# Kernel optimization log

Measured on AMD Instinct MI355X. Metric: run time of the kernel, lower is better.

Reference implementation:

```python
import jax, jax.numpy as jnp
import numpy as np

THRESH = 0.5      # jaccard_thresh
NEGPOS = 3        # neg:pos ratio for hard negative mining
VAR0, VAR1 = 0.1, 0.2  # SSD encoding variances


def point_form(boxes):
    # center-size [P,4] -> (xmin,ymin,xmax,ymax)
    return jnp.concatenate([boxes[:, :2] - boxes[:, 2:] / 2,
                            boxes[:, :2] + boxes[:, 2:] / 2], axis=1)


def jaccard(box_a, box_b):
    # box_a [O,4], box_b [P,4] point-form -> IoU [O,P]
    lt = jnp.maximum(box_a[:, None, :2], box_b[None, :, :2])
    rb = jnp.minimum(box_a[:, None, 2:], box_b[None, :, 2:])
    wh = jnp.clip(rb - lt, 0.0)
    inter = wh[..., 0] * wh[..., 1]
    area_a = ((box_a[:, 2] - box_a[:, 0]) * (box_a[:, 3] - box_a[:, 1]))[:, None]
    area_b = ((box_b[:, 2] - box_b[:, 0]) * (box_b[:, 3] - box_b[:, 1]))[None, :]
    return inter / (area_a + area_b - inter)


def encode(matched, priors):
    # matched point-form [P,4], priors center-size [P,4]
    g_cxcy = ((matched[:, :2] + matched[:, 2:]) / 2 - priors[:, :2]) / (VAR0 * priors[:, 2:])
    g_wh = jnp.log((matched[:, 2:] - matched[:, :2]) / priors[:, 2:]) / VAR1
    return jnp.concatenate([g_cxcy, g_wh], axis=1)


def match_one(truths, labels, priors):
    # truths [O,4] point-form, labels [O] int, priors [P,4] center-size
    O = truths.shape[0]
    ov = jaccard(truths, point_form(priors))          # [O,P]
    best_prior_idx = jnp.argmax(ov, axis=1)           # [O]
    best_truth_ov = jnp.max(ov, axis=0)               # [P]
    best_truth_idx = jnp.argmax(ov, axis=0)           # [P]
    # ensure each gt matches its best prior
    best_truth_ov = best_truth_ov.at[best_prior_idx].set(2.0)
    best_truth_idx = best_truth_idx.at[best_prior_idx].set(jnp.arange(O))
    matches = truths[best_truth_idx]                  # [P,4]
    conf = jnp.where(best_truth_ov < THRESH, 0, labels[best_truth_idx] + 1)
    return encode(matches, priors), conf


def setup_inputs() -> dict:
    key = jax.random.key(0)
    ks = jax.random.split(key, 6)
    B, P, C, O = 32, 24656, 81, 16
    predictions = jax.random.normal(ks[0], (B, P, 4 + C), dtype=jnp.float32)
    # priors: center-size, valid w/h
    pc = jax.random.uniform(ks[1], (P, 2), minval=0.05, maxval=0.95)
    pwh = jax.random.uniform(ks[2], (P, 2), minval=0.02, maxval=0.3)
    priors = jnp.concatenate([pc, pwh], axis=1).astype(jnp.float32)
    # ground-truth boxes in point form, guaranteed positive extent
    tc = jax.random.uniform(ks[3], (B, O, 2), minval=0.2, maxval=0.8)
    twh = jax.random.uniform(ks[4], (B, O, 2), minval=0.05, maxval=0.3)
    targets_boxes = jnp.concatenate([tc - twh / 2, tc + twh / 2], axis=-1).astype(jnp.float32)
    targets_labels = jax.random.randint(ks[5], (B, O), 0, C - 1, dtype=jnp.int32)
    return {"predictions": predictions, "targets_boxes": targets_boxes,
            "targets_labels": targets_labels, "priors": priors}


def reference(predictions, targets_boxes, targets_labels, priors):
    loc_data = predictions[..., :4]        # [B,P,4]
    conf_data = predictions[..., 4:]       # [B,P,C]
    B, P = loc_data.shape[:2]
    C = conf_data.shape[2]

    loc_t, conf_t = jax.vmap(match_one, in_axes=(0, 0, None))(
        targets_boxes, targets_labels, priors)   # [B,P,4], [B,P]

    pos = conf_t > 0                                   # [B,P]
    # smooth L1 on positives, sum reduction
    d = loc_data - loc_t
    ad = jnp.abs(d)
    sl1 = jnp.where(ad < 1.0, 0.5 * d * d, ad - 0.5)
    loss_l = jnp.sum(sl1 * pos[..., None].astype(sl1.dtype))

    # per-anchor cross entropy
    logp = jax.nn.log_softmax(conf_data, axis=-1)
    lbl = jnp.clip(conf_t, 0, C - 1)
    ce = -jnp.take_along_axis(logp, lbl[..., None], axis=-1)[..., 0]  # [B,P]

    # hard negative mining: rank negatives by loss (positives zeroed)
    loss_rank = jnp.where(pos, 0.0, ce)
    loss_idx = jnp.argsort(-loss_rank, axis=1)
    idx_rank = jnp.argsort(loss_idx, axis=1)
    num_pos = jnp.sum(pos, axis=1, keepdims=True)          # [B,1]
    num_neg = jnp.minimum(num_pos * NEGPOS, P)
    neg = idx_rank < num_neg

    sel = (pos | neg).astype(ce.dtype)
    loss_c = jnp.sum(ce * sel)

    N = jnp.sum(num_pos).astype(loss_l.dtype)
    return loss_l / N, loss_c / N
```

## Files before the change

kernel.cpp:

```cpp
#include <hip/hip_runtime.h>
#include <math.h>

#define NB 32
#define NP 24656
#define NO 16
#define NC 81
#define ND 85
#define THRESH_F 0.5f
#define NEGPOS_I 3
#define VAR0_F 0.1f
#define VAR1_F 0.2f
#define NEG_HUGE -1e30f

#define BPCNT (NB * NP)
#define MBLK2 25
#define CHB32 771
#define SPB2 56
#define CB32 11264

typedef unsigned long long u64;

__global__ __launch_bounds__(256) void k_match(
    const float* __restrict__ tboxes, const float* __restrict__ priors,
    u64* __restrict__ mcand,
    int* __restrict__ npos, float* __restrict__ accB, int* __restrict__ done) {
    const int b = blockIdx.y, bx = blockIdx.x, tid = threadIdx.x;
    __shared__ float tb[NO * 4];
    __shared__ u64 kbuf[NO][256];
    __shared__ u64 pbuf[NO][16];
    if (bx == 0 && b == 0) {
        if (tid < NB) npos[tid] = 0;
        if (tid < 2 * NB) accB[tid] = 0.f;
        if (tid == 0) *done = 0;
    }
    if (tid < NO * 4) tb[tid] = tboxes[b * NO * 4 + tid];
    __syncthreads();

    const int p0 = bx * 1024 + tid * 4;
    float pl[4], pt[4], prr[4], pbm[4], pa[4];
    bool pv[4];
#pragma unroll
    for (int j = 0; j < 4; ++j) {
        const int p = p0 + j;
        pv[j] = (p < NP);
        const float4 q = pv[j] ? ((const float4*)priors)[p]
                               : make_float4(0.f, 0.f, 1.f, 1.f);
        pl[j] = q.x - q.z * 0.5f; pt[j] = q.y - q.w * 0.5f;
        prr[j] = q.x + q.z * 0.5f; pbm[j] = q.y + q.w * 0.5f;
        pa[j] = (prr[j] - pl[j]) * (pbm[j] - pt[j]);
    }
    for (int o = 0; o < NO; ++o) {
        const float al = tb[o * 4], at = tb[o * 4 + 1];
        const float ar = tb[o * 4 + 2], ab = tb[o * 4 + 3];
        const float aarea = (ar - al) * (ab - at);
        u64 kmax = 0ull;
#pragma unroll
        for (int j = 0; j < 4; ++j) {
            float iw = fminf(ar, prr[j]) - fmaxf(al, pl[j]); iw = fmaxf(iw, 0.f);
            float ih = fminf(ab, pbm[j]) - fmaxf(at, pt[j]); ih = fmaxf(ih, 0.f);
            const float inter = iw * ih;
            const float iou = inter / (aarea + pa[j] - inter);
            if (pv[j]) {
                const u64 key = ((u64)__float_as_uint(iou) << 32) |
                                (u64)(0xFFFFFFFFu - (unsigned)(p0 + j));
                kmax = (key > kmax) ? key : kmax;
            }
        }
        kbuf[o][tid] = kmax;
    }
    __syncthreads();
    {
        const int o = tid >> 4, seg = tid & 15;
        u64 m = kbuf[o][seg];
#pragma unroll
        for (int i = 1; i < 16; ++i) {
            const u64 v = kbuf[o][i * 16 + seg];
            m = (v > m) ? v : m;
        }
        pbuf[o][seg] = m;
    }
    __syncthreads();
    if (tid < NO) {
        u64 m = pbuf[tid][0];
#pragma unroll
        for (int i = 1; i < 16; ++i) {
            const u64 v = pbuf[tid][i];
            m = (v > m) ? v : m;
        }
        mcand[((size_t)(b * NO + tid)) * MBLK2 + bx] = m;
    }
}

__device__ __forceinline__ void stage_load(float4* vreg,
                                           const char* __restrict__ gpred,
                                           int b, int r0, int lane) {
    const size_t off = ((size_t)b * NP + r0) * 340ull;
    const char* g = gpred + off;
    const bool unsafe = (b == NB - 1) && (r0 + 34 > NP);
    if (!unsafe) {
#pragma unroll
        for (int k = 0; k < 11; ++k)
            vreg[k] = *(const float4*)(g + k * 1024 + lane * 16);
    } else {
        const int nf4 = (NP - r0) * ND / 4;
        const float4* gs = (const float4*)g;
#pragma unroll
        for (int k = 0; k < 11; ++k) {
            const int idx = k * 64 + lane;
            vreg[k] = (idx < nf4) ? gs[idx]
                                  : make_float4(0.f, 0.f, 0.f, 0.f);
        }
    }
}

__device__ __forceinline__ void stage_write(char* buf, const float4* vreg,
                                            int lane) {
#pragma unroll
    for (int k = 0; k < 11; ++k)
        *(float4*)(buf + k * 1024 + lane * 16) = vreg[k];
}

__global__ __launch_bounds__(64) void k_main(
    const float* __restrict__ pred, const float* __restrict__ tboxes,
    const int* __restrict__ tlabels, const float* __restrict__ priors,
    const u64* __restrict__ mcand,
    float* __restrict__ lr, int* __restrict__ npos, float* __restrict__ accB) {
    __shared__ char smem[2][CB32];
    __shared__ float tbs[NO * 4];

    const int b = blockIdx.y;
    const int span = blockIdx.x;
    const int lane = threadIdx.x;
    const size_t bbase = (size_t)b * NP;
    const char* gpred = (const char*)pred;

    char* cur = smem[0];
    char* nxt = smem[1];

    const int rho = lane >> 1;
    const int h = lane & 1;
    const int c0 = rho & 3;
    const int Ab = 16 * (21 * rho + (rho >> 2));
    const int sbase = h ? 11 : 1;

    tbs[lane] = tboxes[b * NO * 4 + lane];

    u64 pbk = 0ull;
    if (lane < NO) {
        const u64* c = mcand + (size_t)(b * NO + lane) * MBLK2;
        for (int i = 0; i < MBLK2; ++i) {
            const u64 v = c[i];
            pbk = (v > pbk) ? v : pbk;
        }
    }
    int p16[NO];
#pragma unroll
    for (int j = 0; j < NO; ++j) {
        const u64 kj = __shfl(pbk, j, 64);
        p16[j] = (int)(0xFFFFFFFFu - (unsigned)(kj & 0xFFFFFFFFull));
    }

    float my_ll = 0.f, my_ce = 0.f;
    int my_np = 0;

    int chunk = span;
    int next_chunk = chunk + SPB2;
    {
        float4 vreg[11];
        stage_load(vreg, gpred, b, chunk * 32, lane);
        stage_write(cur, vreg, lane);
    }

    while (chunk < CHB32) {
        float4 vreg[11];
        const bool have_next = (next_chunk < CHB32);
        if (have_next)
            stage_load(vreg, gpred, b, next_chunk * 32, lane);

        const int r0 = chunk * 32;
        const int nrows = min(32, NP - r0);
        const int p = r0 + rho;
        const bool rok = (rho < nrows);

        float4 v[11];
#pragma unroll
        for (int k = 0; k < 11; ++k)
            v[k] = *(const float4*)(cur + Ab + 16 * (sbase + k));

        float vals[44];
#pragma unroll
        for (int k = 0; k < 11; ++k) {
            const float xs[4] = {v[k].x, v[k].y, v[k].z, v[k].w};
#pragma unroll
            for (int t = 0; t < 4; ++t) {
                bool ok;
                if (k == 0)
                    ok = h ? false : (t >= c0);
                else if (k == 10)
                    ok = h ? (t <= c0) : true;
                else
                    ok = true;
                vals[4 * k + t] = ok ? xs[t] : NEG_HUGE;
            }
        }
        float mA = vals[0], mB = vals[1];
#pragma unroll
        for (int j = 2; j < 44; j += 2) {
            mA = fmaxf(mA, vals[j]);
            mB = fmaxf(mB, vals[j + 1]);
        }
        float m = fmaxf(mA, mB);
        m = fmaxf(m, __shfl_xor(m, 1, 64));

        float sA = 0.f, sB = 0.f;
#pragma unroll
        for (int j = 0; j < 44; j += 2) {
            sA += __expf(vals[j] - m);
            sB += __expf(vals[j + 1] - m);
        }
        float ssum = sA + sB;
        ssum += __shfl_xor(ssum, 1, 64);
        const float lse = m + __logf(ssum);

        float bv = -1.f;
        int bi = 0;
        {
            const float4 pq = rok ? *((const float4*)priors + p)
                                  : make_float4(0.f, 0.f, 1.f, 1.f);
            const float prl = pq.x - pq.z * 0.5f, prt = pq.y - pq.w * 0.5f;
            const float prr2 = pq.x + pq.z * 0.5f, prb = pq.y + pq.w * 0.5f;
            const float parea = (prr2 - prl) * (prb - prt);
            const int obase = h * 8;
#pragma unroll
            for (int oj = 0; oj < 8; ++oj) {
                const int o = obase + oj;
                const float al = tbs[o * 4 + 0], at = tbs[o * 4 + 1];
                const float ar = tbs[o * 4 + 2], ab = tbs[o * 4 + 3];
                float iw = fminf(ar, prr2) - fmaxf(al, prl); iw = fmaxf(iw, 0.f);
                float ih = fminf(ab, prb) - fmaxf(at, prt); ih = fmaxf(ih, 0.f);
                const float inter = iw * ih;
                const float aarea = (ar - al) * (ab - at);
                const float iou = inter / (aarea + parea - inter);
                if (iou > bv) { bv = iou; bi = o; }
            }
            const float ov = __shfl_xor(bv, 1, 64);
            const int oi = __shfl_xor(bi, 1, 64);
            if (ov > bv || (ov == bv && oi < bi)) { bv = ov; bi = oi; }
        }

        if (h == 0 && rok) {
            const float bg = (c0 == 0) ? v[0].x : (c0 == 1) ? v[0].y
                           : (c0 == 2) ? v[0].z : v[0].w;
            int o_f = -1;
#pragma unroll
            for (int j = 0; j < NO; ++j)
                if (p == p16[j]) o_f = j;
            const bool forced = (o_f >= 0);
            const bool pos = forced || (bv >= THRESH_F);
            const int o = forced ? o_f : bi;
            lr[bbase + p] = pos ? 0.f : (lse - bg);
            if (pos) {
                my_np += 1;
                const float* rowp = (const float*)(cur + 340 * rho);
                const int lbl = tlabels[b * NO + o] + 1;
                my_ce += lse - rowp[4 + lbl];
                const float4 pq = *((const float4*)priors + p);
                const float tx0 = tbs[o * 4 + 0];
                const float ty0 = tbs[o * 4 + 1];
                const float tx1 = tbs[o * 4 + 2];
                const float ty1 = tbs[o * 4 + 3];
                const float g0 = ((tx0 + tx1) * 0.5f - pq.x) / (VAR0_F * pq.z);
                const float g1 = ((ty0 + ty1) * 0.5f - pq.y) / (VAR0_F * pq.w);
                const float g2 = __logf((tx1 - tx0) / pq.z) / VAR1_F;
                const float g3 = __logf((ty1 - ty0) / pq.w) / VAR1_F;
                float dd, ad;
                dd = rowp[0] - g0; ad = fabsf(dd); my_ll += (ad < 1.f) ? 0.5f * dd * dd : (ad - 0.5f);
                dd = rowp[1] - g1; ad = fabsf(dd); my_ll += (ad < 1.f) ? 0.5f * dd * dd : (ad - 0.5f);
                dd = rowp[2] - g2; ad = fabsf(dd); my_ll += (ad < 1.f) ? 0.5f * dd * dd : (ad - 0.5f);
                dd = rowp[3] - g3; ad = fabsf(dd); my_ll += (ad < 1.f) ? 0.5f * dd * dd : (ad - 0.5f);
            }
        }

        if (have_next)
            stage_write(nxt, vreg, lane);

        chunk = next_chunk;
        next_chunk += SPB2;
        char* tmp = cur; cur = nxt; nxt = tmp;
    }

    for (int d2 = 1; d2 < 64; d2 <<= 1) {
        my_ll += __shfl_xor(my_ll, d2, 64);
        my_ce += __shfl_xor(my_ce, d2, 64);
        my_np += __shfl_xor(my_np, d2, 64);
    }
    if (lane == 0) {
        if (my_ll != 0.f) atomicAdd(&accB[b * 2 + 0], my_ll);
        if (my_ce != 0.f) atomicAdd(&accB[b * 2 + 1], my_ce);
        if (my_np) atomicAdd(&npos[b], my_np);
    }
}

__global__ __launch_bounds__(1024) void k_select(
    const float* __restrict__ lrk, const int* __restrict__ npos,
    float* __restrict__ accB, int* __restrict__ done, float* __restrict__ out) {
    const int b = blockIdx.x;
    const float4* row4 = (const float4*)(lrk + (size_t)b * NP);
    const int tid = threadIdx.x;
    const int lane = tid & 63;
    const int wid = tid >> 6;
    const int sub = lane & 15;

    __shared__ unsigned hist16[2048][16];
    __shared__ unsigned chist[2048];
    __shared__ int sh_bucket, sh_knew;
    __shared__ float wsum[16];
    __shared__ int wcnt[16];

    float4 cch[7];
    bool cvz[7];
#pragma unroll
    for (int j = 0; j < 7; ++j) {
        const int i = tid + j * 1024;
        cvz[j] = (i < NP / 4);
        cch[j] = cvz[j] ? row4[i] : make_float4(0.f, 0.f, 0.f, 0.f);
    }

    const int K0 = min(npos[b] * NEGPOS_I, NP);
    int k = K0;
    unsigned prefix = 0;

    const int shifts[3] = {21, 10, 0};
    const unsigned masks[3] = {0u, 0xFFE00000u, 0xFFFFFC00u};

    for (int pass = 0; pass < 3; ++pass) {
        const int shift = shifts[pass];
        const unsigned mask_hi = masks[pass];
        {
            uint4* hz = (uint4*)hist16;
            for (int j = tid; j < 2048 * 4; j += 1024)
                hz[j] = make_uint4(0u, 0u, 0u, 0u);
        }
        __syncthreads();
#pragma unroll
        for (int j = 0; j < 7; ++j) {
            if (cvz[j]) {
                const float4 v4 = cch[j];
#pragma unroll
                for (int c = 0; c < 4; ++c) {
                    const float f = (c == 0) ? v4.x : (c == 1) ? v4.y
                                  : (c == 2) ? v4.z : v4.w;
                    const unsigned v = __float_as_uint(f);
                    if ((v & mask_hi) == (prefix & mask_hi))
                        atomicAdd(&hist16[(v >> shift) & 2047u][sub], 1u);
                }
            }
        }
        __syncthreads();
        for (int j = tid; j < 2048; j += 1024) {
            const uint4* hp = (const uint4*)&hist16[j][0];
            const uint4 a = hp[0], b4 = hp[1], c4 = hp[2], d4 = hp[3];
            chist[j] = a.x + a.y + a.z + a.w + b4.x + b4.y + b4.z + b4.w +
                       c4.x + c4.y + c4.z + c4.w + d4.x + d4.y + d4.z + d4.w;
        }
        __syncthreads();
        if (tid < 64) {
            unsigned g = 0;
            for (int j = 0; j < 32; ++j) g += chist[lane * 32 + j];
            unsigned T = g;
            for (int d = 1; d < 64; d <<= 1) {
                const unsigned t = __shfl_down(T, d, 64);
                if (lane + d < 64) T += t;
            }
            const unsigned E = T - g;
            const bool hit = (E < (unsigned)k) && ((unsigned)k <= T);
            const unsigned long long msk = __ballot(hit);
            const int wl = __ffsll(msk) - 1;
            if (lane == wl) {
                unsigned cum = E;
                int bsel = lane * 32, kn = k;
                for (int j = 31; j >= 0; --j) {
                    const unsigned c = chist[lane * 32 + j];
                    if (cum + c >= (unsigned)k) {
                        bsel = lane * 32 + j;
                        kn = k - (int)cum;
                        break;
                    }
                    cum += c;
                }
                sh_bucket = bsel;
                sh_knew = kn;
            }
        }
        __syncthreads();
        prefix |= ((unsigned)sh_bucket) << shift;
        k = sh_knew;
        __syncthreads();
    }
    const float T = __uint_as_float(prefix);

    float msum = 0.f;
    int mcnt = 0;
#pragma unroll
    for (int j = 0; j < 7; ++j) {
        if (cvz[j]) {
            const float4 v4 = cch[j];
#pragma unroll
            for (int c = 0; c < 4; ++c) {
                const float f = (c == 0) ? v4.x : (c == 1) ? v4.y
                              : (c == 2) ? v4.z : v4.w;
                if (__float_as_uint(f) > prefix) { msum += f; mcnt++; }
            }
        }
    }
    for (int s = 32; s > 0; s >>= 1) {
        msum += __shfl_down(msum, s, 64);
        mcnt += __shfl_down(mcnt, s, 64);
    }
    if (lane == 0) { wsum[wid] = msum; wcnt[wid] = mcnt; }
    __syncthreads();
    if (tid == 0) {
        float tot = 0.f;
        int cnt = 0;
        for (int w = 0; w < 16; ++w) { tot += wsum[w]; cnt += wcnt[w]; }
        atomicAdd(&accB[b * 2 + 1], tot + (float)(K0 - cnt) * T);
        __threadfence();
        if (atomicAdd(done, 1) == NB - 1) {
            volatile const float* va = accB;
            volatile const int* vn = npos;
            int n = 0;
            float a0 = 0.f, a1 = 0.f;
            for (int bb = 0; bb < NB; ++bb) {
                n += vn[bb];
                a0 += va[bb * 2 + 0];
                a1 += va[bb * 2 + 1];
            }
            const float N = (float)n;
            out[0] = a0 / N;
            out[1] = a1 / N;
        }
    }
}

extern "C" void kernel_launch(void* const* d_in, const int* in_sizes, int n_in,
                              void* d_out, int out_size, void* d_ws, size_t ws_size,
                              hipStream_t stream) {
    const float* pred   = (const float*)d_in[0];
    const float* tboxes = (const float*)d_in[1];
    const int*   tlabels = (const int*)d_in[2];
    const float* priors = (const float*)d_in[3];
    float* out = (float*)d_out;

    char* w = (char*)d_ws;
    float*  lrk = (float*)(w + 8ull * BPCNT);
    u64*    mcand = (u64*)(w + 12ull * BPCNT);
    char*   w2 = w + 12ull * BPCNT + 8ull * NB * NO * MBLK2;
    int*    npos = (int*)w2;
    float*  accB = (float*)(w2 + 4ull * NB);
    int*    done = (int*)(w2 + 4ull * NB + 8ull * NB);

    k_match<<<dim3(MBLK2, NB), dim3(256), 0, stream>>>(
        tboxes, priors, mcand, npos, accB, done);
    k_main<<<dim3(SPB2, NB), dim3(64), 0, stream>>>(
        pred, tboxes, tlabels, priors, mcand, lrk, npos, accB);
    k_select<<<dim3(NB), dim3(1024), 0, stream>>>(lrk, npos, accB, done, out);
}
```

Baseline: 108.2 us.

## Fold best-prior matching into main pass and correct forced matches in select

Removes the separate k_match kernel. k_main now computes each ground truth's best prior per span alongside its existing IoU work and writes per-span candidates. k_select reduces those candidates and then patches the forced-match corrections: the loss delta for the forced truth, the positive count, and zeroing lrk. Per-batch atomics and the done counter are replaced by per-span partial buffers and a tiny final reduction kernel. This saves one launch and the extra IoU pass, but adds a serial fix-up in k_select, a third single-thread kernel, and extra per-row key-max work in k_main.

```diff
diff --git a/kernel.cpp b/kernel.cpp
--- a/kernel.cpp
+++ b/kernel.cpp
@@ -13,83 +13,11 @@
 #define NEG_HUGE -1e30f
 
 #define BPCNT (NB * NP)
-#define MBLK2 25
 #define CHB32 771
 #define SPB2 56
 #define CB32 11264
 
 typedef unsigned long long u64;
-
-__global__ __launch_bounds__(256) void k_match(
-    const float* __restrict__ tboxes, const float* __restrict__ priors,
-    u64* __restrict__ mcand,
-    int* __restrict__ npos, float* __restrict__ accB, int* __restrict__ done) {
-    const int b = blockIdx.y, bx = blockIdx.x, tid = threadIdx.x;
-    __shared__ float tb[NO * 4];
-    __shared__ u64 kbuf[NO][256];
-    __shared__ u64 pbuf[NO][16];
-    if (bx == 0 && b == 0) {
-        if (tid < NB) npos[tid] = 0;
-        if (tid < 2 * NB) accB[tid] = 0.f;
-        if (tid == 0) *done = 0;
-    }
-    if (tid < NO * 4) tb[tid] = tboxes[b * NO * 4 + tid];
-    __syncthreads();
-
-    const int p0 = bx * 1024 + tid * 4;
-    float pl[4], pt[4], prr[4], pbm[4], pa[4];
-    bool pv[4];
-#pragma unroll
-    for (int j = 0; j < 4; ++j) {
-        const int p = p0 + j;
-        pv[j] = (p < NP);
-        const float4 q = pv[j] ? ((const float4*)priors)[p]
-                               : make_float4(0.f, 0.f, 1.f, 1.f);
-        pl[j] = q.x - q.z * 0.5f; pt[j] = q.y - q.w * 0.5f;
-        prr[j] = q.x + q.z * 0.5f; pbm[j] = q.y + q.w * 0.5f;
-        pa[j] = (prr[j] - pl[j]) * (pbm[j] - pt[j]);
-    }
-    for (int o = 0; o < NO; ++o) {
-        const float al = tb[o * 4], at = tb[o * 4 + 1];
-        const float ar = tb[o * 4 + 2], ab = tb[o * 4 + 3];
-        const float aarea = (ar - al) * (ab - at);
-        u64 kmax = 0ull;
-#pragma unroll
-        for (int j = 0; j < 4; ++j) {
-            float iw = fminf(ar, prr[j]) - fmaxf(al, pl[j]); iw = fmaxf(iw, 0.f);
-            float ih = fminf(ab, pbm[j]) - fmaxf(at, pt[j]); ih = fmaxf(ih, 0.f);
-            const float inter = iw * ih;
-            const float iou = inter / (aarea + pa[j] - inter);
-            if (pv[j]) {
-                const u64 key = ((u64)__float_as_uint(iou) << 32) |
-                                (u64)(0xFFFFFFFFu - (unsigned)(p0 + j));
-                kmax = (key > kmax) ? key : kmax;
-            }
-        }
-        kbuf[o][tid] = kmax;
-    }
-    __syncthreads();
-    {
-        const int o = tid >> 4, seg = tid & 15;
-        u64 m = kbuf[o][seg];
-#pragma unroll
-        for (int i = 1; i < 16; ++i) {
-            const u64 v = kbuf[o][i * 16 + seg];
-            m = (v > m) ? v : m;
-        }
-        pbuf[o][seg] = m;
-    }
-    __syncthreads();
-    if (tid < NO) {
-        u64 m = pbuf[tid][0];
-#pragma unroll
-        for (int i = 1; i < 16; ++i) {
-            const u64 v = pbuf[tid][i];
-            m = (v > m) ? v : m;
-        }
-        mcand[((size_t)(b * NO + tid)) * MBLK2 + bx] = m;
-    }
-}
 
 __device__ __forceinline__ void stage_load(float4* vreg,
                                            const char* __restrict__ gpred,
@@ -120,13 +48,33 @@
         *(float4*)(buf + k * 1024 + lane * 16) = vreg[k];
 }
 
+__device__ __forceinline__ float sl1enc(const float l0, const float l1,
+                                        const float l2, const float l3,
+                                        const float4 pq,
+                                        const float* __restrict__ tb4) {
+    const float tx0 = tb4[0], ty0 = tb4[1], tx1 = tb4[2], ty1 = tb4[3];
+    const float g0 = ((tx0 + tx1) * 0.5f - pq.x) / (VAR0_F * pq.z);
+    const float g1 = ((ty0 + ty1) * 0.5f - pq.y) / (VAR0_F * pq.w);
+    const float g2 = __logf((tx1 - tx0) / pq.z) / VAR1_F;
+    const float g3 = __logf((ty1 - ty0) / pq.w) / VAR1_F;
+    float s = 0.f, dd, ad;
+    dd = l0 - g0; ad = fabsf(dd); s += (ad < 1.f) ? 0.5f * dd * dd : (ad - 0.5f);
+    dd = l1 - g1; ad = fabsf(dd); s += (ad < 1.f) ? 0.5f * dd * dd : (ad - 0.5f);
+    dd = l2 - g2; ad = fabsf(dd); s += (ad < 1.f) ? 0.5f * dd * dd : (ad - 0.5f);
+    dd = l3 - g3; ad = fabsf(dd); s += (ad < 1.f) ? 0.5f * dd * dd : (ad - 0.5f);
+    return s;
+}
+
 __global__ __launch_bounds__(64) void k_main(
     const float* __restrict__ pred, const float* __restrict__ tboxes,
     const int* __restrict__ tlabels, const float* __restrict__ priors,
-    const u64* __restrict__ mcand,
-    float* __restrict__ lr, int* __restrict__ npos, float* __restrict__ accB) {
+    float* __restrict__ lr, u64* __restrict__ bcand,
+    float* __restrict__ pll, float* __restrict__ pce,
+    float* __restrict__ pnp) {
     __shared__ char smem[2][CB32];
     __shared__ float tbs[NO * 4];
+    __shared__ u64 kk[16][32];
+    __shared__ u64 pb2[16][4];
 
     const int b = blockIdx.y;
     const int span = blockIdx.x;
@@ -145,20 +93,9 @@
 
     tbs[lane] = tboxes[b * NO * 4 + lane];
 
-    u64 pbk = 0ull;
-    if (lane < NO) {
-        const u64* c = mcand + (size_t)(b * NO + lane) * MBLK2;
-        for (int i = 0; i < MBLK2; ++i) {
-            const u64 v = c[i];
-            pbk = (v > pbk) ? v : pbk;
-        }
-    }
-    int p16[NO];
-#pragma unroll
-    for (int j = 0; j < NO; ++j) {
-        const u64 kj = __shfl(pbk, j, 64);
-        p16[j] = (int)(0xFFFFFFFFu - (unsigned)(kj & 0xFFFFFFFFull));
-    }
+    u64 ok[8];
+#pragma unroll
+    for (int j = 0; j < 8; ++j) ok[j] = 0ull;
 
     float my_ll = 0.f, my_ce = 0.f;
     int my_np = 0;
@@ -193,14 +130,14 @@
             const float xs[4] = {v[k].x, v[k].y, v[k].z, v[k].w};
 #pragma unroll
             for (int t = 0; t < 4; ++t) {
-                bool ok;
+                bool okv;
                 if (k == 0)
-                    ok = h ? false : (t >= c0);
+                    okv = h ? false : (t >= c0);
                 else if (k == 10)
-                    ok = h ? (t <= c0) : true;
+                    okv = h ? (t <= c0) : true;
                 else
-                    ok = true;
-                vals[4 * k + t] = ok ? xs[t] : NEG_HUGE;
+                    okv = true;
+                vals[4 * k + t] = okv ? xs[t] : NEG_HUGE;
             }
         }
         float mA = vals[0], mB = vals[1];
@@ -242,6 +179,11 @@
                 const float aarea = (ar - al) * (ab - at);
                 const float iou = inter / (aarea + parea - inter);
                 if (iou > bv) { bv = iou; bi = o; }
+                if (rok) {
+                    const u64 key = ((u64)__float_as_uint(iou) << 32) |
+                                    (u64)(0xFFFFFFFFu - (unsigned)p);
+                    ok[oj] = (key > ok[oj]) ? key : ok[oj];
+                }
             }
             const float ov = __shfl_xor(bv, 1, 64);
             const int oi = __shfl_xor(bi, 1, 64);
@@ -251,13 +193,8 @@
         if (h == 0 && rok) {
             const float bg = (c0 == 0) ? v[0].x : (c0 == 1) ? v[0].y
                            : (c0 == 2) ? v[0].z : v[0].w;
-            int o_f = -1;
-#pragma unroll
-            for (int j = 0; j < NO; ++j)
-                if (p == p16[j]) o_f = j;
-            const bool forced = (o_f >= 0);
-            const bool pos = forced || (bv >= THRESH_F);
-            const int o = forced ? o_f : bi;
+            const bool pos = (bv >= THRESH_F);
+            const int o = bi;
             lr[bbase + p] = pos ? 0.f : (lse - bg);
             if (pos) {
                 my_np += 1;
@@ -265,19 +202,8 @@
                 const int lbl = tlabels[b * NO + o] + 1;
                 my_ce += lse - rowp[4 + lbl];
                 const float4 pq = *((const float4*)priors + p);
-                const float tx0 = tbs[o * 4 + 0];
-                const float ty0 = tbs[o * 4 + 1];
-                const float tx1 = tbs[o * 4 + 2];
-                const float ty1 = tbs[o * 4 + 3];
-                const float g0 = ((tx0 + tx1) * 0.5f - pq.x) / (VAR0_F * pq.z);
-                const float g1 = ((ty0 + ty1) * 0.5f - pq.y) / (VAR0_F * pq.w);
-                const float g2 = __logf((tx1 - tx0) / pq.z) / VAR1_F;
-                const float g3 = __logf((ty1 - ty0) / pq.w) / VAR1_F;
-                float dd, ad;
-                dd = rowp[0] - g0; ad = fabsf(dd); my_ll += (ad < 1.f) ? 0.5f * dd * dd : (ad - 0.5f);
-                dd = rowp[1] - g1; ad = fabsf(dd); my_ll += (ad < 1.f) ? 0.5f * dd * dd : (ad - 0.5f);
-                dd = rowp[2] - g2; ad = fabsf(dd); my_ll += (ad < 1.f) ? 0.5f * dd * dd : (ad - 0.5f);
-                dd = rowp[3] - g3; ad = fabsf(dd); my_ll += (ad < 1.f) ? 0.5f * dd * dd : (ad - 0.5f);
+                my_ll += sl1enc(rowp[0], rowp[1], rowp[2], rowp[3], pq,
+                                &tbs[o * 4]);
             }
         }
 
@@ -295,17 +221,43 @@
         my_np += __shfl_xor(my_np, d2, 64);
     }
     if (lane == 0) {
-        if (my_ll != 0.f) atomicAdd(&accB[b * 2 + 0], my_ll);
-        if (my_ce != 0.f) atomicAdd(&accB[b * 2 + 1], my_ce);
-        if (my_np) atomicAdd(&npos[b], my_np);
+        pll[b * SPB2 + span] = my_ll;
+        pce[b * SPB2 + span] = my_ce;
+        pnp[b * SPB2 + span] = (float)my_np;
+    }
+
+#pragma unroll
+    for (int j = 0; j < 8; ++j) kk[h * 8 + j][rho] = ok[j];
+    __syncthreads();
+    {
+        const int o = lane >> 2, seg = lane & 3;
+        u64 m2 = 0ull;
+#pragma unroll
+        for (int i = 0; i < 8; ++i) {
+            const u64 vv = kk[o][seg * 8 + i];
+            m2 = (vv > m2) ? vv : m2;
+        }
+        pb2[o][seg] = m2;
+    }
+    __syncthreads();
+    if (lane < NO) {
+        u64 m2 = pb2[lane][0];
+#pragma unroll
+        for (int i = 1; i < 4; ++i) {
+            const u64 vv = pb2[lane][i];
+            m2 = (vv > m2) ? vv : m2;
+        }
+        bcand[((size_t)b * NO + lane) * SPB2 + span] = m2;
     }
 }
 
 __global__ __launch_bounds__(1024) void k_select(
-    const float* __restrict__ lrk, const int* __restrict__ npos,
-    float* __restrict__ accB, int* __restrict__ done, float* __restrict__ out) {
+    const float* __restrict__ pred, const float* __restrict__ tboxes,
+    const int* __restrict__ tlabels, const float* __restrict__ priors,
+    float* __restrict__ lrk, const u64* __restrict__ bcand,
+    const float* __restrict__ pll, const float* __restrict__ pce,
+    const float* __restrict__ pnp, float* __restrict__ pout) {
     const int b = blockIdx.x;
-    const float4* row4 = (const float4*)(lrk + (size_t)b * NP);
     const int tid = threadIdx.x;
     const int lane = tid & 63;
     const int wid = tid >> 6;
@@ -316,7 +268,148 @@
     __shared__ int sh_bucket, sh_knew;
     __shared__ float wsum[16];
     __shared__ int wcnt[16];
-
+    __shared__ float tbs[NO * 4];
+    __shared__ int tl[NO];
+    __shared__ u64 pbq[16][4];
+    __shared__ int p16s[16];
+    __shared__ float sparts[56 * 3];
+    __shared__ float sll, sce, snp_f;
+    __shared__ float fll, fce;
+    __shared__ int fnp;
+
+    if (tid < NO * 4) tbs[tid] = tboxes[b * NO * 4 + tid];
+    if (tid >= 128 && tid < 128 + NO) tl[tid - 128] = tlabels[b * NO + tid - 128];
+    if (tid < 64) {
+        const int o = tid & 15, grp = tid >> 4;
+        const u64* c = bcand + ((size_t)b * NO + o) * SPB2 + grp * 14;
+        u64 m = 0ull;
+        for (int i = 0; i < 14; ++i) {
+            const u64 v = c[i];
+            m = (v > m) ? v : m;
+        }
+        pbq[o][grp] = m;
+    }
+    if (tid >= 64 && tid < 120) {
+        const int l = tid - 64;
+        sparts[l * 3 + 0] = pll[b * SPB2 + l];
+        sparts[l * 3 + 1] = pce[b * SPB2 + l];
+        sparts[l * 3 + 2] = pnp[b * SPB2 + l];
+    }
+    __syncthreads();
+    if (tid < NO) {
+        u64 m = pbq[tid][0];
+#pragma unroll
+        for (int i = 1; i < 4; ++i) {
+            const u64 v = pbq[tid][i];
+            m = (v > m) ? v : m;
+        }
+        p16s[tid] = (int)(0xFFFFFFFFu - (unsigned)(m & 0xFFFFFFFFull));
+    }
+    if (tid == 32) {
+        float a = 0.f, c = 0.f, n = 0.f;
+        for (int l = 0; l < 56; ++l) {
+            a += sparts[l * 3 + 0];
+            c += sparts[l * 3 + 1];
+            n += sparts[l * 3 + 2];
+        }
+        sll = a; sce = c; snp_f = n;
+    }
+    __syncthreads();
+    if (tid < 64) {
+        const int g = lane >> 2, q = lane & 3;
+        const int p = p16s[g];
+        bool winner = true;
+        for (int o2 = g + 1; o2 < NO; ++o2)
+            if (p16s[o2] == p) winner = false;
+        float dll = 0.f, dce = 0.f;
+        int dnp = 0;
+        if (winner) {
+            const float* base = pred + (size_t)b * NP * ND;
+            const int A = 21 * p + (p >> 2), c0 = p & 3;
+            const float4* vp = (const float4*)base + A;
+            float vals[24];
+#pragma unroll
+            for (int k = 0; k < 6; ++k) {
+                const int s = q + 4 * k;
+                const float4 f4 = vp[(s <= 21) ? s : 21];
+                const float xs[4] = {f4.x, f4.y, f4.z, f4.w};
+#pragma unroll
+                for (int t = 0; t < 4; ++t) {
+                    const int d = 4 * s + t - c0;
+                    vals[4 * k + t] =
+                        (s <= 21 && d >= 4 && d <= 84) ? xs[t] : NEG_HUGE;
+                }
+            }
+            float mx = vals[0];
+#pragma unroll
+            for (int j = 1; j < 24; ++j) mx = fmaxf(mx, vals[j]);
+            mx = fmaxf(mx, __shfl_xor(mx, 1, 64));
+            mx = fmaxf(mx, __shfl_xor(mx, 2, 64));
+            float es = 0.f;
+#pragma unroll
+            for (int j = 0; j < 24; ++j) es += __expf(vals[j] - mx);
+            es += __shfl_xor(es, 1, 64);
+            es += __shfl_xor(es, 2, 64);
+            const float lse = mx + __logf(es);
+            const float4 pq = *((const float4*)priors + p);
+            const float prl = pq.x - pq.z * 0.5f, prt = pq.y - pq.w * 0.5f;
+            const float prr2 = pq.x + pq.z * 0.5f, prb = pq.y + pq.w * 0.5f;
+            const float parea = (prr2 - prl) * (prb - prt);
+            float bv = -1.f;
+            int bi = 0;
+#pragma unroll
+            for (int jj = 0; jj < 4; ++jj) {
+                const int o2 = q * 4 + jj;
+                const float al = tbs[o2 * 4 + 0], at = tbs[o2 * 4 + 1];
+                const float ar = tbs[o2 * 4 + 2], ab = tbs[o2 * 4 + 3];
+                float iw = fminf(ar, prr2) - fmaxf(al, prl); iw = fmaxf(iw, 0.f);
+                float ih = fminf(ab, prb) - fmaxf(at, prt); ih = fmaxf(ih, 0.f);
+                const float inter = iw * ih;
+                const float aarea = (ar - al) * (ab - at);
+                const float iou = inter / (aarea + parea - inter);
+                if (iou > bv) { bv = iou; bi = o2; }
+            }
+#pragma unroll
+            for (int d = 1; d <= 2; d <<= 1) {
+                const float ov = __shfl_xor(bv, d, 64);
+                const int oi = __shfl_xor(bi, d, 64);
+                if (ov > bv || (ov == bv && oi < bi)) { bv = ov; bi = oi; }
+            }
+            if (q == 0) {
+                const float* rowp = base + (size_t)p * ND;
+                const float l0 = rowp[0], l1 = rowp[1];
+                const float l2 = rowp[2], l3 = rowp[3];
+                const bool was_pos = (bv >= THRESH_F);
+                const float ce_f = lse - rowp[4 + tl[g] + 1];
+                const float ll_f = sl1enc(l0, l1, l2, l3, pq, &tbs[g * 4]);
+                if (was_pos) {
+                    const float ce_nf = lse - rowp[4 + tl[bi] + 1];
+                    const float ll_nf = sl1enc(l0, l1, l2, l3, pq, &tbs[bi * 4]);
+                    dll = ll_f - ll_nf;
+                    dce = ce_f - ce_nf;
+                } else {
+                    dll = ll_f;
+                    dce = ce_f;
+                    dnp = 1;
+                    lrk[(size_t)b * NP + p] = 0.f;
+                }
+            }
+        }
+        for (int d2 = 1; d2 < 64; d2 <<= 1) {
+            dll += __shfl_xor(dll, d2, 64);
+            dce += __shfl_xor(dce, d2, 64);
+            dnp += __shfl_xor(dnp, d2, 64);
+        }
+        if (lane == 0) { fll = dll; fce = dce; fnp = dnp; }
+    }
+    __threadfence_block();
+    __syncthreads();
+
+    const float llb = sll + fll;
+    const float ceb = sce + fce;
+    const int npb = (int)(snp_f + 0.5f) + fnp;
+
+    const float4* row4 = (const float4*)(lrk + (size_t)b * NP);
     float4 cch[7];
     bool cvz[7];
 #pragma unroll
@@ -326,10 +419,9 @@
         cch[j] = cvz[j] ? row4[i] : make_float4(0.f, 0.f, 0.f, 0.f);
     }
 
-    const int K0 = min(npos[b] * NEGPOS_I, NP);
+    const int K0 = min(npb * NEGPOS_I, NP);
     int k = K0;
     unsigned prefix = 0;
-
     const int shifts[3] = {21, 10, 0};
     const unsigned masks[3] = {0u, 0xFFE00000u, 0xFFFFFC00u};
 
@@ -423,22 +515,24 @@
         float tot = 0.f;
         int cnt = 0;
         for (int w = 0; w < 16; ++w) { tot += wsum[w]; cnt += wcnt[w]; }
-        atomicAdd(&accB[b * 2 + 1], tot + (float)(K0 - cnt) * T);
-        __threadfence();
-        if (atomicAdd(done, 1) == NB - 1) {
-            volatile const float* va = accB;
-            volatile const int* vn = npos;
-            int n = 0;
-            float a0 = 0.f, a1 = 0.f;
-            for (int bb = 0; bb < NB; ++bb) {
-                n += vn[bb];
-                a0 += va[bb * 2 + 0];
-                a1 += va[bb * 2 + 1];
-            }
-            const float N = (float)n;
-            out[0] = a0 / N;
-            out[1] = a1 / N;
-        }
+        const float negsum = tot + (float)(K0 - cnt) * T;
+        pout[b * 4 + 0] = llb;
+        pout[b * 4 + 1] = ceb + negsum;
+        pout[b * 4 + 2] = (float)npb;
+    }
+}
+
+__global__ void k_final(const float* __restrict__ pout,
+                        float* __restrict__ out) {
+    if (threadIdx.x == 0 && blockIdx.x == 0) {
+        float a0 = 0.f, a1 = 0.f, n = 0.f;
+        for (int b = 0; b < NB; ++b) {
+            a0 += pout[b * 4 + 0];
+            a1 += pout[b * 4 + 1];
+            n += pout[b * 4 + 2];
+        }
+        out[0] = a0 / n;
+        out[1] = a1 / n;
     }
 }
 
@@ -452,16 +546,17 @@
     float* out = (float*)d_out;
 
     char* w = (char*)d_ws;
-    float*  lrk = (float*)(w + 8ull * BPCNT);
-    u64*    mcand = (u64*)(w + 12ull * BPCNT);
-    char*   w2 = w + 12ull * BPCNT + 8ull * NB * NO * MBLK2;
-    int*    npos = (int*)w2;
-    float*  accB = (float*)(w2 + 4ull * NB);
-    int*    done = (int*)(w2 + 4ull * NB + 8ull * NB);
-
-    k_match<<<dim3(MBLK2, NB), dim3(256), 0, stream>>>(
-        tboxes, priors, mcand, npos, accB, done);
+    float* lrk  = (float*)w;
+    u64*   bcand = (u64*)(w + 4ull * BPCNT);
+    char*  w2 = w + 4ull * BPCNT + 8ull * NB * NO * SPB2;
+    float* pll = (float*)w2;
+    float* pce = (float*)(w2 + 4ull * NB * SPB2);
+    float* pnp = (float*)(w2 + 8ull * NB * SPB2);
+    float* pout = (float*)(w2 + 12ull * NB * SPB2);
+
     k_main<<<dim3(SPB2, NB), dim3(64), 0, stream>>>(
-        pred, tboxes, tlabels, priors, mcand, lrk, npos, accB);
-    k_select<<<dim3(NB), dim3(1024), 0, stream>>>(lrk, npos, accB, done, out);
-}
+        pred, tboxes, tlabels, priors, lrk, bcand, pll, pce, pnp);
+    k_select<<<dim3(NB), dim3(1024), 0, stream>>>(
+        pred, tboxes, tlabels, priors, lrk, bcand, pll, pce, pnp, pout);
+    k_final<<<dim3(1), dim3(1), 0, stream>>>(pout, out);
+}
```

Result: faster. 104.7 us, median of 2 (-3.1%).
